# Performance work log

Measured on AMD Instinct MI355X. Metric: run time of the kernel, lower is better.

## Reference

```python
import jax, jax.numpy as jnp
import numpy as np

MAX_REL = 7  # maxRelativeDist

def _rel_pos_table(L, max_rel):
    # |i-j|, with distances beyond max_rel mapped to max_rel + log2(d - max_rel), clipped to [0, 2*max_rel]
    idx = jnp.arange(L)
    d = jnp.abs(idx[:, None] - idx[None, :]).astype(jnp.float32)
    far = d > max_rel
    d = jnp.where(far, max_rel + jnp.log2(jnp.maximum(d - max_rel, 1.0)), d)
    return jnp.clip(d, 0, 2 * max_rel).astype(jnp.int32)  # [L, L]

def setup_inputs() -> dict:
    key = jax.random.key(0)
    ks = jax.random.split(key, 16)
    B, L, C, P, H, DK = 8, 2048, 512, 64, 8, 64
    s = 0.02
    inp = {
        'qx': jax.random.normal(ks[0], (B, L, C), jnp.float32),
        'kx': jax.random.normal(ks[1], (B, L, C), jnp.float32),
        'vx': jax.random.normal(ks[2], (B, L, C), jnp.float32),
        'maskPAD': jnp.ones((B, L, L), jnp.int32),
        # pseudoAttn: Linear(C, P)
        'Wp': jax.random.normal(ks[3], (C, P), jnp.float32) * s,
        'bp': jnp.zeros((P,), jnp.float32),
        # WQ/WK: Linear(C, dkEnhance*DK*H) with dkEnhance=1
        'Wq': jax.random.normal(ks[4], (C, H * DK), jnp.float32) * s,
        'bq': jnp.zeros((H * DK,), jnp.float32),
        'Wk': jax.random.normal(ks[5], (C, H * DK), jnp.float32) * s,
        'bk': jnp.zeros((H * DK,), jnp.float32),
        'Wv': jax.random.normal(ks[6], (C, H * DK), jnp.float32) * s,
        'bv': jnp.zeros((H * DK,), jnp.float32),
        'Wo': jax.random.normal(ks[7], (H * DK, C), jnp.float32) * s,
        'bo': jnp.zeros((C,), jnp.float32),
        # relative position embeddings: [2*MAX_REL+1, H]
        'embK': jax.random.normal(ks[8], (2 * MAX_REL + 1, H), jnp.float32) * s,
        'embB': jax.random.normal(ks[9], (2 * MAX_REL + 1, H), jnp.float32) * s,
    }
    return inp

def reference(qx, kx, vx, maskPAD, Wp, bp, Wq, bq, Wk, bk, Wv, bv, Wo, bo, embK, embB):
    # dropout is identity (eval mode); preScores=None
    B, L, C = qx.shape
    H = embK.shape[1]
    DK = Wv.shape[1] // H
    P = Wp.shape[1]

    # pseudo-token compression
    pScore = vx @ Wp + bp                                   # [B, L, P]
    mask = (maskPAD[:, 0] == 0)[:, :, None]                 # [B, L, 1]
    pScore = jnp.where(mask, jnp.float32(-2.0 ** 15), pScore)
    pAlpha = jax.nn.softmax(pScore, axis=1)                 # softmax over L
    kxc = jnp.einsum('blp,blc->bpc', pAlpha, kx)            # [B, P, C]
    vxc = jnp.einsum('blp,blc->bpc', pAlpha, vx)            # [B, P, C]
    pAlpha_d = jax.lax.stop_gradient(pAlpha)

    # multi-head projections
    q = (qx @ Wq + bq).reshape(B, L, H, DK)                 # [B, L, H, DK]
    k = (kxc @ Wk + bk).reshape(B, P, H, DK)
    v = (vxc @ Wv + bv).reshape(B, P, H, DK)

    scores = jnp.einsum('blhd,bphd->bhlp', q, k) / np.sqrt(DK)  # [B, H, L, P]

    # relative-position modulation
    relTab = _rel_pos_table(L, MAX_REL)                     # [L, L] int
    Kmat = jnp.transpose(embK[relTab], (2, 1, 0))           # [H, L, L]
    Bmat = jnp.transpose(embB[relTab], (2, 1, 0))           # [H, L, L]
    Kterm = jnp.einsum('hlm,bmp->bhlp', Kmat, pAlpha_d)
    Bterm = jnp.einsum('hlm,bmp->bhlp', Bmat, pAlpha_d)
    scores = scores * Kterm + Bterm

    alpha = jax.nn.softmax(scores, axis=3)                  # over pseudo tokens
    z = jnp.einsum('bhlp,bphd->blhd', alpha, v).reshape(B, L, H * DK)
    z = z @ Wo + bo                                         # [B, L, C]
    return z, pScore, scores
```

## Files before the change

### kernel.cpp

```cpp
#include <hip/hip_runtime.h>


typedef __attribute__((ext_vector_type(8))) short bhalf8;
typedef __attribute__((ext_vector_type(4))) float fx4;

__device__ __forceinline__ unsigned short f2bf(float f) {
  union { float f; unsigned u; } v; v.f = f;
  unsigned u = v.u + 0x7fffu + ((v.u >> 16) & 1u);
  return (unsigned short)(u >> 16);
}
__device__ __forceinline__ float bf2f(unsigned short h) {
  union { unsigned u; float f; } v; v.u = ((unsigned)h) << 16;
  return v.f;
}
__device__ __forceinline__ void gld16(const void* g, void* l) {
  __builtin_amdgcn_global_load_lds(
      (const __attribute__((address_space(1))) void*)g,
      (__attribute__((address_space(3))) void*)l, 16, 0, 0);
}

template <int BM, int BN, int CMODE, int AF32, int KSPLIT, int BF32>
__device__ __forceinline__ void gemm_body(
    int bxx, int byy, int bzz, char* smemc,
    const void* __restrict__ Av, const unsigned short* __restrict__ BT,
    const float* __restrict__ bias, void* __restrict__ Cout,
    int K, int lda, int ldbt, int ldc, int HDIV,
    long sAb, long sAh, long sBb, long sBh, long sCb, long sCh, long sCk,
    const int* __restrict__ mpad, float* __restrict__ aux,
    const float* __restrict__ Bf32, const float* __restrict__ Bf32b)
{
  constexpr int NA = BM / 16, NB = BN / 16, NT = NA + NB;
  constexpr int WM = BM / 2, WN = BN / 2, FM = WM / 16, FN = WN / 16;
  unsigned short* lds = (unsigned short*)smemc;
  const int t = threadIdx.x, l = t & 63, w = t >> 6;
  const int wr = w >> 1, wc = w & 1;
  const int zz = bzz, b = zz / HDIV, h = zz % HDIV;
  const int row0 = KSPLIT ? 0 : byy * BM;
  const int koff = KSPLIT ? byy * K : 0;
  const long cko = KSPLIT ? (long)byy * sCk : 0;
  const int col0 = bxx * BN;
  const unsigned short* Ag = (const unsigned short*)Av + b * sAb + h * sAh + (long)row0 * lda + koff;
  const float* AgF = (const float*)Av + b * sAb + h * sAh + (long)row0 * lda + koff;
  const unsigned short* Bg = BT + b * sBb + h * sBh + (long)col0 * ldbt + koff;
  const int lr = l & 15, lc = l >> 4;

  fx4 acc[FM][FN];
#pragma unroll
  for (int i = 0; i < FM; ++i)
#pragma unroll
    for (int j = 0; j < FN; ++j) acc[i][j] = fx4{0.f, 0.f, 0.f, 0.f};

  for (int k0 = 0; k0 < K; k0 += 32) {
#pragma unroll
    for (int i = 0; i < NT / 4; ++i) {
      const int tile = w + i * 4;
      if (tile < NA) {
        if constexpr (AF32 == 1) {
          const float* gf = AgF + (long)(tile * 16 + lr) * lda + k0 + lc * 8;
          float4 x = *(const float4*)gf, y = *(const float4*)(gf + 4);
          bhalf8 pk;
          pk[0] = (short)f2bf(x.x); pk[1] = (short)f2bf(x.y);
          pk[2] = (short)f2bf(x.z); pk[3] = (short)f2bf(x.w);
          pk[4] = (short)f2bf(y.x); pk[5] = (short)f2bf(y.y);
          pk[6] = (short)f2bf(y.z); pk[7] = (short)f2bf(y.w);
          *(bhalf8*)&lds[tile * 512 + l * 8] = pk;
        } else if constexpr (AF32 == 2) {
          const float* gf = (const float*)Av + (long)zz * sAb + (long)byy * 131072
                            + (long)(tile * 16 + lr) * 512 + k0 + lc * 8;
          float4 x = make_float4(0.f, 0.f, 0.f, 0.f), y = x;
#pragma unroll
          for (int c = 0; c < 4; ++c) {
            float4 a = *(const float4*)(gf + (long)c * 32768);
            float4 bq = *(const float4*)(gf + (long)c * 32768 + 4);
            x.x += a.x; x.y += a.y; x.z += a.z; x.w += a.w;
            y.x += bq.x; y.y += bq.y; y.z += bq.z; y.w += bq.w;
          }
          bhalf8 pk;
          pk[0] = (short)f2bf(x.x); pk[1] = (short)f2bf(x.y);
          pk[2] = (short)f2bf(x.z); pk[3] = (short)f2bf(x.w);
          pk[4] = (short)f2bf(y.x); pk[5] = (short)f2bf(y.y);
          pk[6] = (short)f2bf(y.z); pk[7] = (short)f2bf(y.w);
          *(bhalf8*)&lds[tile * 512 + l * 8] = pk;
        } else {
          gld16(Ag + (long)(tile * 16 + lr) * lda + k0 + lc * 8, &lds[tile * 512]);
        }
      } else {
        if constexpr (BF32 == 1) {
          const int ct = tile - NA;
          const float* gfB = Bf32 + (long)(koff + k0 + lc * 8) * ldbt + col0 + ct * 16 + lr;
          bhalf8 pk;
#pragma unroll
          for (int i2 = 0; i2 < 8; ++i2) pk[i2] = (short)f2bf(gfB[(long)i2 * ldbt]);
          *(bhalf8*)&lds[tile * 512 + l * 8] = pk;
        } else if constexpr (BF32 == 2) {
          const int ct = tile - NA;
          const float* src = (h ? Bf32b : Bf32) + (long)b * 1048576
                             + (long)(koff + k0 + lc * 8) * ldbt + col0 + ct * 16 + lr;
          bhalf8 pk;
#pragma unroll
          for (int i2 = 0; i2 < 8; ++i2) pk[i2] = (short)f2bf(src[(long)i2 * ldbt]);
          *(bhalf8*)&lds[tile * 512 + l * 8] = pk;
        } else {
          gld16(Bg + (long)((tile - NA) * 16 + lr) * ldbt + k0 + lc * 8, &lds[tile * 512]);
        }
      }
    }
    __syncthreads();
    bhalf8 af[FM], bf[FN];
#pragma unroll
    for (int i = 0; i < FM; ++i) af[i] = *(const bhalf8*)&lds[(wr * FM + i) * 512 + l * 8];
#pragma unroll
    for (int j = 0; j < FN; ++j) bf[j] = *(const bhalf8*)&lds[(NA + wc * FN + j) * 512 + l * 8];
#pragma unroll
    for (int i = 0; i < FM; ++i)
#pragma unroll
      for (int j = 0; j < FN; ++j)
        acc[i][j] = __builtin_amdgcn_mfma_f32_16x16x32_bf16(af[i], bf[j], acc[i][j], 0, 0, 0);
    __syncthreads();
  }

  if constexpr (CMODE == 3) {
    float (*tbuf)[65] = (float(*)[65])(smemc + NT * 1024);
#pragma unroll
    for (int fm = 0; fm < FM; ++fm) {
#pragma unroll
      for (int fn = 0; fn < FN; ++fn) {
        const int rg0 = row0 + wr * WM + fm * 16 + lc * 4;
        const int cg = col0 + wc * WN + fn * 16 + lr;
        const float bb = bias[cg];
#pragma unroll
        for (int jj = 0; jj < 4; ++jj) {
          const int rg = rg0 + jj;
          float vv = acc[fm][fn][jj] + bb;
          if (mpad[((long)(rg >> 11)) * (2048L * 2048) + (rg & 2047)] == 0) vv = -32768.f;
          __builtin_nontemporal_store(vv, (float*)Cout + (long)rg * ldc + cg);
          tbuf[rg - row0][cg] = vv;
        }
      }
    }
    __syncthreads();
    const int b0 = row0 >> 11, l0b = row0 & 2047;
    const int pp = t >> 2, li0 = (t & 3) * 16;
    float* dst = aux + ((long)b0 * 64 + pp) * 2048 + l0b + li0;
#pragma unroll
    for (int i = 0; i < 16; i += 4) {
      float4 o = make_float4(tbuf[li0 + i][pp],     tbuf[li0 + i + 1][pp],
                             tbuf[li0 + i + 2][pp], tbuf[li0 + i + 3][pp]);
      *(float4*)(dst + i) = o;
    }
  } else {
#pragma unroll
    for (int fm = 0; fm < FM; ++fm) {
#pragma unroll
      for (int fn = 0; fn < FN; ++fn) {
        const int rg0 = row0 + wr * WM + fm * 16 + lc * 4;
        const int cg = col0 + wc * WN + fn * 16 + lr;
        float bb = 0.f;
        if constexpr (CMODE == 4) {
          bb = (zz == 0) ? bias[cg] : ((const float*)mpad)[cg];
        } else {
          bb = bias ? bias[cg] : 0.f;
        }
#pragma unroll
        for (int jj = 0; jj < 4; ++jj) {
          const int rg = rg0 + jj;
          const float v = acc[fm][fn][jj] + bb;
          if constexpr (CMODE == 0) {
            ((float*)Cout)[b * sCb + h * sCh + cko + (long)rg * ldc + cg] = v;
          } else if constexpr (CMODE == 1) {
            ((unsigned short*)Cout)[b * sCb + h * sCh + (long)rg * ldc + cg] = f2bf(v);
          } else if constexpr (CMODE == 2) {
            ((unsigned short*)Cout)[(((long)(rg >> 6) * 8 + (cg >> 6)) * 64 + (cg & 63)) * 64 + (rg & 63)] = f2bf(v);
          } else if constexpr (CMODE == 4) {
            if (zz == 0)
              ((unsigned short*)Cout)[(long)rg * ldc + cg] = f2bf(v);
            else
              ((unsigned short*)Cout)[262144 + (((long)(rg >> 6) * 8 + (cg >> 6)) * 64 + (cg & 63)) * 64 + (rg & 63)] = f2bf(v);
          } else {
            __builtin_nontemporal_store(v, (float*)Cout + b * sCb + h * sCh + cko + (long)rg * ldc + cg);
          }
        }
      }
    }
  }
}

template <int BM, int BN, int CMODE, int AF32, int KSPLIT>
__global__ __launch_bounds__(256)
void gemm_mfma(const void* __restrict__ Av, const unsigned short* __restrict__ BT,
               const float* __restrict__ bias, void* __restrict__ Cout,
               int K, int lda, int ldbt, int ldc, int HDIV,
               long sAb, long sAh, long sBb, long sBh, long sCb, long sCh, long sCk,
               const int* __restrict__ mpad, float* __restrict__ aux)
{
  constexpr int SM = (BM / 16 + BN / 16) * 1024 + (CMODE == 3 ? 16640 : 0);
  __shared__ __align__(16) char smem[SM];
  gemm_body<BM, BN, CMODE, AF32, KSPLIT, 0>(blockIdx.x, blockIdx.y, blockIdx.z, smem,
      Av, BT, bias, Cout, K, lda, ldbt, ldc, HDIV,
      sAb, sAh, sBb, sBh, sCb, sCh, sCk, mpad, aux, nullptr, nullptr);
}

__device__ __forceinline__ void tr_body(float (*tile)[65], const float* __restrict__ in,
                                        unsigned short* __restrict__ out,
                                        int R, int Cd, int r0, int c0, int t)
{
  const int tr = t >> 4, tc4 = (t & 15) * 4;
#pragma unroll
  for (int pass = 0; pass < 4; ++pass) {
    int r = pass * 16 + tr;
    float4 v = *(const float4*)(in + (long)(r0 + r) * Cd + c0 + tc4);
    tile[r][tc4] = v.x; tile[r][tc4 + 1] = v.y; tile[r][tc4 + 2] = v.z; tile[r][tc4 + 3] = v.w;
  }
  __syncthreads();
#pragma unroll
  for (int pass = 0; pass < 4; ++pass) {
    int c = pass * 16 + tr;
    ushort4 o;
    o.x = f2bf(tile[tc4][c]);     o.y = f2bf(tile[tc4 + 1][c]);
    o.z = f2bf(tile[tc4 + 2][c]); o.w = f2bf(tile[tc4 + 3][c]);
    *(ushort4*)(out + (long)(c0 + c) * R + r0 + tc4) = o;
  }
}

__global__ __launch_bounds__(256)
void combo0(const float* __restrict__ vx, const float* __restrict__ Wp,
            const float* __restrict__ bp, const int* __restrict__ maskPAD,
            float* __restrict__ ps_out, float* __restrict__ pScoreT,
            const float* __restrict__ Wq, const float* __restrict__ Wk,
            const float* __restrict__ Wv, const float* __restrict__ Wo,
            unsigned short* __restrict__ WqT, unsigned short* __restrict__ WkT,
            unsigned short* __restrict__ WvT, unsigned short* __restrict__ WoT)
{
  __shared__ __align__(16) char smem[24832];
  const int id = blockIdx.x;
  if (id < 256) {
    gemm_body<64, 64, 3, 1, 0, 1>(0, id, 0, smem,
        vx, nullptr, bp, ps_out, 512, 512, 64, 64, 1,
        0, 0, 0, 0, 0, 0, 0, maskPAD, pScoreT, Wp, nullptr);
  } else {
    const int r = id - 256;
    const int z = r >> 6, rem = r & 63;
    const float* in; unsigned short* out;
    switch (z) {
      case 0: in = Wq; out = WqT; break;
      case 1: in = Wk; out = WkT; break;
      case 2: in = Wv; out = WvT; break;
      default: in = Wo; out = WoT; break;
    }
    tr_body((float(*)[65])smem, in, out, 512, 512, (rem >> 3) * 64, (rem & 7) * 64, threadIdx.x);
  }
}

__device__ __forceinline__ void kb_body(int bx, int by, char* smemc,
    const unsigned short* __restrict__ PSb,
    const float* __restrict__ embK, const float* __restrict__ embB,
    ushort2* __restrict__ KB)
{
  const int L = 2048, STR = 338;
  unsigned short* psw = (unsigned short*)smemc;
  float (*eKs)[8] = (float(*)[8])(smemc + 43264);
  float (*eBs)[8] = (float(*)[8])(smemc + 43264 + 512);
  const int t = threadIdx.x, b = by, l0 = bx * 64;
  if (t < 128) {
    int r = t >> 3, h = t & 7;
    eKs[r][h] = (r < 15) ? embK[r * 8 + h] : 0.f;
    eBs[r][h] = (r < 15) ? embB[r * 8 + h] : 0.f;
  }
  const int W0 = l0 - 136;
  const int w = t >> 6, ln = t & 63;
  for (int pr = w * 16; pr < w * 16 + 16; ++pr) {
    const unsigned short* src = PSb + ((long)b * 64 + pr) * 2048;
#pragma unroll
    for (int pass = 0; pass < 6; ++pass) {
      int j = pass * 64 + ln;
      if (j < 337) {
        int g = (j == 336) ? (L - 1) : (W0 + j);
        g = g < 0 ? 0 : (g > L - 1 ? L - 1 : g);
        psw[pr * STR + j] = src[g];
      }
    }
  }
  __syncthreads();
  const int p = ln;
  const int Btab[14] = {0,1,2,3,4,5,6,8,10,14,22,38,70,134};
  for (int step = 0; step < 16; ++step) {
    const int l = l0 + w * 16 + step;
    float U[15];
#pragma unroll
    for (int r = 0; r < 14; ++r) {
      int hi = l + Btab[r]; hi = hi > L - 1 ? L - 1 : hi;
      float u = bf2f(psw[p * STR + (hi - W0)]);
      const int lo = l - 1 - Btab[r];
      if (lo >= 0) u -= bf2f(psw[p * STR + (lo - W0)]);
      U[r] = u;
    }
    U[14] = bf2f(psw[p * STR + 336]);
    for (int h = 0; h < 8; ++h) {
      float Kt = 0.f, Bt = 0.f;
#pragma unroll
      for (int r = 0; r < 15; ++r) {
        Kt = fmaf(eKs[r][h] - eKs[r + 1][h], U[r], Kt);
        Bt = fmaf(eBs[r][h] - eBs[r + 1][h], U[r], Bt);
      }
      ushort2 o; o.x = f2bf(Kt); o.y = f2bf(Bt);
      KB[(((long)(b * 8 + h)) * L + l) * 64 + p] = o;
    }
  }
}

__global__ __launch_bounds__(256)
void combo1(const unsigned short* __restrict__ pAbf,
            const float* __restrict__ kx, const float* __restrict__ vx,
            float* __restrict__ pbuf,
            const unsigned short* __restrict__ PSb,
            const float* __restrict__ embK, const float* __restrict__ embB,
            ushort2* __restrict__ KB)
{
  __shared__ __align__(16) char smem[44544];
  const int id = blockIdx.x;
  if (id < 512) {
    gemm_body<64, 64, 0, 0, 1, 2>(id & 7, (id >> 3) & 3, id >> 5, smem,
        pAbf, nullptr, nullptr, pbuf, 512, 2048, 512, 512, 2,
        131072, 0, 0, 0, 131072, 1048576, 32768, nullptr, nullptr, kx, vx);
  } else {
    const int r = id - 512;
    kb_body(r & 31, r >> 5, smem, PSb, embK, embB, KB);
  }
}

__global__ __launch_bounds__(256)
void combo2(const float* __restrict__ pbuf, const unsigned short* __restrict__ WkT,
            const float* __restrict__ bk, const float* __restrict__ bv,
            unsigned short* __restrict__ kp,
            const float* __restrict__ qx, const unsigned short* __restrict__ WqT,
            const float* __restrict__ bq, unsigned short* __restrict__ qbf)
{
  __shared__ __align__(16) char smem[16384];
  const int id = blockIdx.x;
  if (id < 64) {
    gemm_body<64, 128, 4, 2, 0, 0>(id & 3, (id >> 2) & 7, id >> 5, smem,
        pbuf, WkT, bk, kp, 512, 512, 512, 512, 1,
        1048576, 0, 262144, 0, 0, 0, 0, (const int*)bv, nullptr, nullptr, nullptr);
  } else {
    const int r = id - 64;
    gemm_body<128, 128, 1, 1, 0, 0>(r & 3, r >> 2, 0, smem,
        qx, WqT, bq, qbf, 512, 512, 512, 512, 1,
        0, 0, 0, 0, 0, 0, 0, nullptr, nullptr, nullptr, nullptr);
  }
}

__global__ __launch_bounds__(256)
void softmax_scan(const float* __restrict__ pScoreT,
                  unsigned short* __restrict__ PSb, unsigned short* __restrict__ pA_bf)
{
  __shared__ float red[256];
  const int p = blockIdx.x, b = blockIdx.y, t = threadIdx.x;
  const float* row = pScoreT + ((size_t)b * 64 + p) * 2048;
  float4 va = ((const float4*)row)[t * 2], vb = ((const float4*)row)[t * 2 + 1];
  float v[8] = {va.x, va.y, va.z, va.w, vb.x, vb.y, vb.z, vb.w};
  float mx = v[0];
#pragma unroll
  for (int i = 1; i < 8; ++i) mx = fmaxf(mx, v[i]);
  red[t] = mx; __syncthreads();
  for (int s = 128; s > 0; s >>= 1) { if (t < s) red[t] = fmaxf(red[t], red[t + s]); __syncthreads(); }
  float m = red[0]; __syncthreads();
  float e[8]; float s = 0.f;
#pragma unroll
  for (int i = 0; i < 8; ++i) { e[i] = expf(v[i] - m); s += e[i]; }
  red[t] = s; __syncthreads();
  for (int o = 1; o < 256; o <<= 1) {
    float x = (t >= o) ? red[t - o] : 0.f;
    __syncthreads(); red[t] += x; __syncthreads();
  }
  float inv = 1.0f / red[255];
  float run = red[t] - s;
  size_t base = ((size_t)b * 64 + p) * 2048 + (size_t)t * 8;
#pragma unroll
  for (int i = 0; i < 8; ++i) {
    run += e[i];
    PSb[base + i] = f2bf(run * inv);
    pA_bf[base + i] = f2bf(e[i] * inv);
  }
}

__global__ __launch_bounds__(256)
void attn_fused(const unsigned short* __restrict__ qb,
                const unsigned short* __restrict__ kp,
                const unsigned short* __restrict__ vpT,
                const ushort2* __restrict__ KB,
                float* __restrict__ sc_out,
                unsigned short* __restrict__ zpre)
{
  const int L = 2048;
  __shared__ __align__(16) unsigned short stg[24 * 512];
  unsigned short* qkb = &stg[8 * 512];
  const int t = threadIdx.x, l = t & 63, w = t >> 6, lr = l & 15, lc = l >> 4;
  const int flat = blockIdx.y * 16 + blockIdx.x;
  const int swz = (flat & 7) * 128 + (flat >> 3);
  const int z = swz >> 4, b = z >> 3, h = z & 7;
  const int l0 = (swz & 15) * 128;
  const unsigned short* Ag = qb + ((long)(b * L + l0)) * 512 + h * 64;
  const unsigned short* Bg = kp + (long)b * 64 * 512 + h * 64;
#pragma unroll
  for (int i = 0; i < 6; ++i) {
    const int tile = w + i * 4;
    const unsigned short* g;
    if (tile < 16) { int rt = tile >> 1, ks = tile & 1; g = Ag + (long)(rt * 16 + lr) * 512 + ks * 32 + lc * 8; }
    else { int j = tile - 16; int rt = j >> 1, ks = j & 1; g = Bg + (long)(rt * 16 + lr) * 512 + ks * 32 + lc * 8; }
    gld16(g, &stg[tile * 512]);
  }
  const ushort2* kbb = KB + (((long)(b * 8 + h)) * L + l0) * 64 + l;
  unsigned int kbreg[32];
#pragma unroll
  for (int i = 0; i < 32; ++i)
    kbreg[i] = *(const unsigned int*)(kbb + ((long)(w * 32 + i)) * 64);
  __syncthreads();
  const int wr = w >> 1, wc = w & 1;
  fx4 acc[4][2];
#pragma unroll
  for (int i = 0; i < 4; ++i)
#pragma unroll
    for (int j = 0; j < 2; ++j) acc[i][j] = fx4{0.f, 0.f, 0.f, 0.f};
#pragma unroll
  for (int ks = 0; ks < 2; ++ks) {
    bhalf8 af[4], bf[2];
#pragma unroll
    for (int i = 0; i < 4; ++i) af[i] = *(const bhalf8*)&stg[((wr * 4 + i) * 2 + ks) * 512 + l * 8];
#pragma unroll
    for (int j = 0; j < 2; ++j) bf[j] = *(const bhalf8*)&stg[(16 + (wc * 2 + j) * 2 + ks) * 512 + l * 8];
#pragma unroll
    for (int i = 0; i < 4; ++i)
#pragma unroll
      for (int j = 0; j < 2; ++j)
        acc[i][j] = __builtin_amdgcn_mfma_f32_16x16x32_bf16(af[i], bf[j], acc[i][j], 0, 0, 0);
  }
  __syncthreads();
#pragma unroll
  for (int fm = 0; fm < 4; ++fm)
#pragma unroll
    for (int fn = 0; fn < 2; ++fn)
#pragma unroll
      for (int jj = 0; jj < 4; ++jj) {
        const int row = wr * 64 + fm * 16 + lc * 4 + jj;
        const int col = wc * 32 + fn * 16 + lr;
        *(unsigned short*)((char*)qkb + ((row * 128 + col * 2) ^ ((row & 7) << 4))) = f2bf(acc[fm][fn][jj]);
      }
  __syncthreads();
  {
    const unsigned short* Vg = vpT + ((long)(b * 8 + h)) * 64 * 64;
#pragma unroll
    for (int i = 0; i < 2; ++i) {
      const int tile = w + i * 4, rt = tile >> 1, ks = tile & 1;
      gld16(Vg + (long)(rt * 16 + lr) * 64 + ks * 32 + lc * 8, &stg[tile * 512]);
    }
  }
  const int p = l;
  float* scb = sc_out + ((long)(b * 8 + h) * L + l0) * 64 + p;
#pragma unroll
  for (int c = 0; c < 8; ++c) {
    const int rbase = w * 32 + c * 4;
    float sv[4];
#pragma unroll
    for (int il = 0; il < 4; ++il) {
      const int row = rbase + il;
      const unsigned int kbw = kbreg[c * 4 + il];
      const float qkv = bf2f(*(const unsigned short*)((const char*)qkb + ((row * 128 + p * 2) ^ ((row & 7) << 4))));
      sv[il] = qkv * 0.125f * bf2f((unsigned short)(kbw & 0xffffu)) + bf2f((unsigned short)(kbw >> 16));
      __builtin_nontemporal_store(sv[il], scb + (long)row * 64);
    }
    float mx[4] = {sv[0], sv[1], sv[2], sv[3]};
#pragma unroll
    for (int o = 32; o > 0; o >>= 1)
#pragma unroll
      for (int il = 0; il < 4; ++il) mx[il] = fmaxf(mx[il], __shfl_xor(mx[il], o, 64));
    float ex[4], sm[4];
#pragma unroll
    for (int il = 0; il < 4; ++il) { ex[il] = __expf(sv[il] - mx[il]); sm[il] = ex[il]; }
#pragma unroll
    for (int o = 32; o > 0; o >>= 1)
#pragma unroll
      for (int il = 0; il < 4; ++il) sm[il] += __shfl_xor(sm[il], o, 64);
#pragma unroll
    for (int il = 0; il < 4; ++il) {
      const int row = rbase + il;
      *(unsigned short*)((char*)qkb + ((row * 128 + p * 2) ^ ((row & 7) << 4))) = f2bf(ex[il] / sm[il]);
    }
  }
  __syncthreads();
  fx4 a2[4][2];
#pragma unroll
  for (int i = 0; i < 4; ++i)
#pragma unroll
    for (int j = 0; j < 2; ++j) a2[i][j] = fx4{0.f, 0.f, 0.f, 0.f};
#pragma unroll
  for (int ks = 0; ks < 2; ++ks) {
    bhalf8 paf[4], pvf[2];
#pragma unroll
    for (int i = 0; i < 4; ++i) {
      const int row = (wr * 4 + i) * 16 + lr;
      paf[i] = *(const bhalf8*)((const char*)qkb + ((row * 128 + ks * 64 + lc * 16) ^ ((row & 7) << 4)));
    }
#pragma unroll
    for (int j = 0; j < 2; ++j)
      pvf[j] = *(const bhalf8*)&stg[(((wc * 2 + j) * 2 + ks) * 512) + l * 8];
#pragma unroll
    for (int i = 0; i < 4; ++i)
#pragma unroll
      for (int j = 0; j < 2; ++j)
        a2[i][j] = __builtin_amdgcn_mfma_f32_16x16x32_bf16(paf[i], pvf[j], a2[i][j], 0, 0, 0);
  }
#pragma unroll
  for (int fm = 0; fm < 4; ++fm)
#pragma unroll
    for (int fn = 0; fn < 2; ++fn)
#pragma unroll
      for (int jj = 0; jj < 4; ++jj) {
        const int row = wr * 64 + fm * 16 + lc * 4 + jj;
        const int col = wc * 32 + fn * 16 + lr;
        zpre[((long)(b * L + l0 + row)) * 512 + h * 64 + col] = f2bf(a2[fm][fn][jj]);
      }
}

extern "C" void kernel_launch(void* const* d_in, const int* in_sizes, int n_in,
                              void* d_out, int out_size, void* d_ws, size_t ws_size,
                              hipStream_t stream)
{
  const int B = 8, L = 2048, C = 512, P = 64;
  const float* qx = (const float*)d_in[0];
  const float* kx = (const float*)d_in[1];
  const float* vx = (const float*)d_in[2];
  const int* maskPAD = (const int*)d_in[3];
  const float* Wp = (const float*)d_in[4];
  const float* bp = (const float*)d_in[5];
  const float* Wq = (const float*)d_in[6];
  const float* bq = (const float*)d_in[7];
  const float* Wk = (const float*)d_in[8];
  const float* bk = (const float*)d_in[9];
  const float* Wv = (const float*)d_in[10];
  const float* bv = (const float*)d_in[11];
  const float* Wo = (const float*)d_in[12];
  const float* bo = (const float*)d_in[13];
  const float* embK = (const float*)d_in[14];
  const float* embB = (const float*)d_in[15];

  float* z_out  = (float*)d_out;
  float* ps_out = z_out + (size_t)B * L * C;
  float* sc_out = ps_out + (size_t)B * L * P;

  char* w8 = (char*)d_ws;
  size_t o = 0;
  auto take = [&](size_t n) { char* r = w8 + o; o += n; return r; };
  unsigned short* R_A  = (unsigned short*)take(16777216);
  unsigned short* R_B  = (unsigned short*)take(16777216);
  unsigned short* WqT  = (unsigned short*)take(524288);
  unsigned short* WkT  = (unsigned short*)take(524288);
  unsigned short* WvT  = (unsigned short*)take(524288);
  unsigned short* WoT  = (unsigned short*)take(524288);
  float* pScoreT       = (float*)take(4194304);
  unsigned short* PSb  = (unsigned short*)take(2097152);
  unsigned short* pAbf = (unsigned short*)take(2097152);
  float* pbuf          = (float*)take(8388608);
  unsigned short* kp   = (unsigned short*)take(1048576);
  ushort2* KB          = (ushort2*)take(33554432);

  combo0<<<dim3(512), 256, 0, stream>>>(
      vx, Wp, bp, maskPAD, ps_out, pScoreT,
      Wq, Wk, Wv, Wo, WqT, WkT, WvT, WoT);
  softmax_scan<<<dim3(P, B), 256, 0, stream>>>(pScoreT, PSb, pAbf);
  combo1<<<dim3(768), 256, 0, stream>>>(pAbf, kx, vx, pbuf, PSb, embK, embB, KB);
  combo2<<<dim3(576), 256, 0, stream>>>(pbuf, WkT, bk, bv, kp, qx, WqT, bq, R_B);
  attn_fused<<<dim3(16, 64), 256, 0, stream>>>(
      R_B, kp, kp + 262144, KB, sc_out, R_A);
  gemm_mfma<128, 128, 5, 0, 0><<<dim3(4, 128, 1), 256, 0, stream>>>(
      R_A, WoT, bo, z_out, 512, 512, 512, 512, 1, 0, 0, 0, 0, 0, 0, 0, nullptr, nullptr);
}
```

Measured before the change: 198.3 us.

## Store prefix-sum transposed and read it directly from global in kb_body

softmax_scan now writes the cumulative pAlpha prefix sums in an [B, L, P] layout instead of [B, P, L]. kb_body can then read the 64 pseudo-token values for each position with coalesced global loads, so the LDS staging window and its barrier-bound fill loop are dropped. The kb grid is split into four times as many smaller blocks, and combo1's shared memory shrinks from 44544 to 8192 bytes, which should raise occupancy. In exchange, softmax_scan's prefix-sum stores become strided 2-byte writes, and kb_body loads repeated window elements from cache instead of LDS.

```diff
diff --git a/kernel.cpp b/kernel.cpp
--- a/kernel.cpp
+++ b/kernel.cpp
@@ -252,49 +252,37 @@
 }
 
 __device__ __forceinline__ void kb_body(int bx, int by, char* smemc,
-    const unsigned short* __restrict__ PSb,
+    const unsigned short* __restrict__ PST,
     const float* __restrict__ embK, const float* __restrict__ embB,
     ushort2* __restrict__ KB)
 {
-  const int L = 2048, STR = 338;
-  unsigned short* psw = (unsigned short*)smemc;
-  float (*eKs)[8] = (float(*)[8])(smemc + 43264);
-  float (*eBs)[8] = (float(*)[8])(smemc + 43264 + 512);
-  const int t = threadIdx.x, b = by, l0 = bx * 64;
+  const int L = 2048;
+  float (*eKs)[8] = (float(*)[8])smemc;
+  float (*eBs)[8] = (float(*)[8])(smemc + 512);
+  const int t = threadIdx.x, b = by, l0 = bx * 16;
   if (t < 128) {
     int r = t >> 3, h = t & 7;
     eKs[r][h] = (r < 15) ? embK[r * 8 + h] : 0.f;
     eBs[r][h] = (r < 15) ? embB[r * 8 + h] : 0.f;
   }
-  const int W0 = l0 - 136;
-  const int w = t >> 6, ln = t & 63;
-  for (int pr = w * 16; pr < w * 16 + 16; ++pr) {
-    const unsigned short* src = PSb + ((long)b * 64 + pr) * 2048;
-#pragma unroll
-    for (int pass = 0; pass < 6; ++pass) {
-      int j = pass * 64 + ln;
-      if (j < 337) {
-        int g = (j == 336) ? (L - 1) : (W0 + j);
-        g = g < 0 ? 0 : (g > L - 1 ? L - 1 : g);
-        psw[pr * STR + j] = src[g];
-      }
-    }
-  }
   __syncthreads();
-  const int p = ln;
+  const int p = t & 63, lw = t >> 6;
   const int Btab[14] = {0,1,2,3,4,5,6,8,10,14,22,38,70,134};
-  for (int step = 0; step < 16; ++step) {
-    const int l = l0 + w * 16 + step;
+  const unsigned short* pst = PST + (long)b * L * 64 + p;
+  const float u2047 = bf2f(pst[(long)(L - 1) * 64]);
+#pragma unroll
+  for (int il = 0; il < 4; ++il) {
+    const int l = l0 + lw * 4 + il;
     float U[15];
 #pragma unroll
     for (int r = 0; r < 14; ++r) {
       int hi = l + Btab[r]; hi = hi > L - 1 ? L - 1 : hi;
-      float u = bf2f(psw[p * STR + (hi - W0)]);
+      float u = bf2f(pst[(long)hi * 64]);
       const int lo = l - 1 - Btab[r];
-      if (lo >= 0) u -= bf2f(psw[p * STR + (lo - W0)]);
+      if (lo >= 0) u -= bf2f(pst[(long)lo * 64]);
       U[r] = u;
     }
-    U[14] = bf2f(psw[p * STR + 336]);
+    U[14] = u2047;
     for (int h = 0; h < 8; ++h) {
       float Kt = 0.f, Bt = 0.f;
 #pragma unroll
@@ -312,11 +300,11 @@
 void combo1(const unsigned short* __restrict__ pAbf,
             const float* __restrict__ kx, const float* __restrict__ vx,
             float* __restrict__ pbuf,
-            const unsigned short* __restrict__ PSb,
+            const unsigned short* __restrict__ PST,
             const float* __restrict__ embK, const float* __restrict__ embB,
             ushort2* __restrict__ KB)
 {
-  __shared__ __align__(16) char smem[44544];
+  __shared__ __align__(16) char smem[8192];
   const int id = blockIdx.x;
   if (id < 512) {
     gemm_body<64, 64, 0, 0, 1, 2>(id & 7, (id >> 3) & 3, id >> 5, smem,
@@ -324,7 +312,7 @@
         131072, 0, 0, 0, 131072, 1048576, 32768, nullptr, nullptr, kx, vx);
   } else {
     const int r = id - 512;
-    kb_body(r & 31, r >> 5, smem, PSb, embK, embB, KB);
+    kb_body(r & 127, r >> 7, smem, PST, embK, embB, KB);
   }
 }
 
@@ -351,7 +339,7 @@
 
 __global__ __launch_bounds__(256)
 void softmax_scan(const float* __restrict__ pScoreT,
-                  unsigned short* __restrict__ PSb, unsigned short* __restrict__ pA_bf)
+                  unsigned short* __restrict__ PST, unsigned short* __restrict__ pA_bf)
 {
   __shared__ float red[256];
   const int p = blockIdx.x, b = blockIdx.y, t = threadIdx.x;
@@ -374,12 +362,13 @@
   }
   float inv = 1.0f / red[255];
   float run = red[t] - s;
-  size_t base = ((size_t)b * 64 + p) * 2048 + (size_t)t * 8;
+  size_t baseA = ((size_t)b * 64 + p) * 2048 + (size_t)t * 8;
+  size_t baseT = ((size_t)b * 2048 + (size_t)t * 8) * 64 + p;
 #pragma unroll
   for (int i = 0; i < 8; ++i) {
     run += e[i];
-    PSb[base + i] = f2bf(run * inv);
-    pA_bf[base + i] = f2bf(e[i] * inv);
+    PST[baseT + (size_t)i * 64] = f2bf(run * inv);
+    pA_bf[baseA + i] = f2bf(e[i] * inv);
   }
 }
 
@@ -557,7 +546,7 @@
   unsigned short* WvT  = (unsigned short*)take(524288);
   unsigned short* WoT  = (unsigned short*)take(524288);
   float* pScoreT       = (float*)take(4194304);
-  unsigned short* PSb  = (unsigned short*)take(2097152);
+  unsigned short* PST  = (unsigned short*)take(2097152);
   unsigned short* pAbf = (unsigned short*)take(2097152);
   float* pbuf          = (float*)take(8388608);
   unsigned short* kp   = (unsigned short*)take(1048576);
@@ -566,8 +555,8 @@
   combo0<<<dim3(512), 256, 0, stream>>>(
       vx, Wp, bp, maskPAD, ps_out, pScoreT,
       Wq, Wk, Wv, Wo, WqT, WkT, WvT, WoT);
-  softmax_scan<<<dim3(P, B), 256, 0, stream>>>(pScoreT, PSb, pAbf);
-  combo1<<<dim3(768), 256, 0, stream>>>(pAbf, kx, vx, pbuf, PSb, embK, embB, KB);
+  softmax_scan<<<dim3(P, B), 256, 0, stream>>>(pScoreT, PST, pAbf);
+  combo1<<<dim3(1536), 256, 0, stream>>>(pAbf, kx, vx, pbuf, PST, embK, embB, KB);
   combo2<<<dim3(576), 256, 0, stream>>>(pbuf, WkT, bk, bv, kp, qx, WqT, bq, R_B);
   attn_fused<<<dim3(16, 64), 256, 0, stream>>>(
       R_B, kp, kp + 262144, KB, sc_out, R_A);
```

New measurement: 259.7 us. +31.0%, slower.
